# Performance work log

Measured on AMD Instinct MI355X. Metric: run time of the kernel, lower is better.

The kernel has to match this reference:

```python
import jax, jax.numpy as jnp
import numpy as np


def setup_inputs() -> dict:
    key = jax.random.key(0)
    kx, ky = jax.random.split(key)
    x = jax.random.normal(kx, (4, 8192, 3), dtype=jnp.float32)
    y = jax.random.normal(ky, (4, 8192, 3), dtype=jnp.float32)
    return {"x": x, "y": y}


def _chamfer(x, y):
    # x: [B, N, D], y: [B, M, D]
    x2 = jnp.sum(x * x, axis=-1)                      # [B, N]
    y2 = jnp.sum(y * y, axis=-1)                      # [B, M]
    xy = jnp.einsum("bnd,bmd->bnm", x, y)             # [B, N, M]
    d2 = x2[:, :, None] + y2[:, None, :] - 2.0 * xy   # [B, N, M]
    d2 = jnp.maximum(d2, 0.0)
    cham_x = jnp.min(d2, axis=2).mean(axis=1)         # [B] min over M, mean over N
    cham_y = jnp.min(d2, axis=1).mean(axis=1)         # [B] min over N, mean over M
    return cham_x + cham_y                            # [B]


def reference(x, y):
    per_batch = _chamfer(x, y)
    return jnp.mean(per_batch)  # batch_reduction='mean'
```

## Files before the change

kernel.cpp:

```cpp
#include <hip/hip_runtime.h>


#define N_      8192
#define NGRP    128
#define FLT_BIG 3.0e38f

typedef float v2f __attribute__((ext_vector_type(2)));

__global__ void zero_out_kernel(float* out) { *out = 0.0f; }

static __device__ __forceinline__ void do_record_v(
    v2f pxs, v2f pys, v2f pzs, v2f wv,
    const v2f* qx, const v2f* qy, const v2f* qz,
    float* acc)
{
    #pragma unroll
    for (int j = 0; j < 4; ++j) {
        v2f td, ts;
        asm("v_pk_fma_f32 %0, %1, %2, %3"
            : "=v"(td) : "v"(qz[j]), "v"(pzs), "v"(wv));
        asm("v_pk_fma_f32 %0, %1, %2, %3 op_sel:[0,1,1] op_sel_hi:[1,0,0]"
            : "=v"(ts) : "v"(qz[j]), "v"(pzs), "v"(wv));
        asm("v_pk_fma_f32 %0, %1, %2, %0"
            : "+v"(td) : "v"(qy[j]), "v"(pys));
        asm("v_pk_fma_f32 %0, %1, %2, %0 op_sel:[0,1,0] op_sel_hi:[1,0,1]"
            : "+v"(ts) : "v"(qy[j]), "v"(pys));
        asm("v_pk_fma_f32 %0, %1, %2, %0"
            : "+v"(td) : "v"(qx[j]), "v"(pxs));
        asm("v_pk_fma_f32 %0, %1, %2, %0 op_sel:[0,1,0] op_sel_hi:[1,0,1]"
            : "+v"(ts) : "v"(qx[j]), "v"(pxs));
        asm("v_min3_f32 %0, %0, %1, %2" : "+v"(acc[2*j])   : "v"(td.x), "v"(ts.x));
        asm("v_min3_f32 %0, %0, %1, %2" : "+v"(acc[2*j+1]) : "v"(td.y), "v"(ts.y));
    }
}

__global__ __launch_bounds__(512, 4) void chamfer_kernel(
    const float* __restrict__ xraw, const float* __restrict__ yraw,
    float* __restrict__ partial,
    unsigned int* __restrict__ ctrl,
    float* __restrict__ out)
{
    __shared__ float4 recs4[2048];
    __shared__ float  red[8 * 512];
    __shared__ unsigned int sflag;

    const int tid  = threadIdx.x;
    const int lane = tid & 63;
    const int wave = __builtin_amdgcn_readfirstlane(tid >> 6);
    const int blk  = blockIdx.x;
    const int dir   = blk >> 8;
    const int batch = (blk >> 6) & 3;
    const int qg    = (blk >> 2) & 15;
    const int seg   = blk & 3;
    const int g     = blk >> 2;

    const float* qraw = dir ? yraw : xraw;
    const float* oraw = dir ? xraw : yraw;

    {
        const float4* src4 =
            (const float4*)(oraw + (size_t)(batch * N_ + seg * 2048) * 3) + tid * 3;
        float4 a = src4[0], b = src4[1], c = src4[2];
        float w00 = fmaf(a.x, a.x, fmaf(a.y, a.y, a.z * a.z));
        float w01 = fmaf(a.w, a.w, fmaf(b.x, b.x, b.y * b.y));
        float w10 = fmaf(b.z, b.z, fmaf(b.w, b.w, c.x * c.x));
        float w11 = fmaf(c.y, c.y, fmaf(c.z, c.z, c.w * c.w));
        float4* d = &recs4[tid * 4];
        d[0] = make_float4(a.x, a.w, a.y, b.x);
        d[1] = make_float4(a.z, b.y, w00, w01);
        d[2] = make_float4(b.z, c.y, b.w, c.z);
        d[3] = make_float4(c.x, c.w, w10, w11);
    }

    const int qbase = batch * N_ + qg * 512;
    float f[24];
    {
        const float4* qv = (const float4*)(qraw + (size_t)qbase * 3) + lane * 6;
        #pragma unroll
        for (int k = 0; k < 6; ++k) {
            float4 t = qv[k];
            f[4*k] = t.x; f[4*k+1] = t.y; f[4*k+2] = t.z; f[4*k+3] = t.w;
        }
    }
    v2f qx[4], qy[4], qz[4];
    float acc[8];
    #pragma unroll
    for (int j = 0; j < 4; ++j) {
        qx[j] = (v2f){-2.0f * f[6*j+0], -2.0f * f[6*j+3]};
        qy[j] = (v2f){-2.0f * f[6*j+1], -2.0f * f[6*j+4]};
        qz[j] = (v2f){-2.0f * f[6*j+2], -2.0f * f[6*j+5]};
        acc[2*j] = FLT_BIG; acc[2*j+1] = FLT_BIG;
    }
    __syncthreads();

    const float* rp = (const float*)&recs4[wave * 256];
    #pragma unroll 4
    for (int k = 0; k < 128; ++k) {
        v2f pxs = *(const v2f*)(rp + k * 8 + 0);
        v2f pys = *(const v2f*)(rp + k * 8 + 2);
        v2f pzs = *(const v2f*)(rp + k * 8 + 4);
        v2f wv  = *(const v2f*)(rp + k * 8 + 6);
        do_record_v(pxs, pys, pzs, wv, qx, qy, qz, acc);
    }

    #pragma unroll
    for (int j = 0; j < 8; ++j) red[wave * 512 + lane * 8 + j] = acc[j];
    __syncthreads();
    float m = red[tid];
    #pragma unroll
    for (int w = 1; w < 8; ++w) m = fminf(m, red[w * 512 + tid]);

    partial[((size_t)g * 4 + seg) * 512 + tid] = m;
    __syncthreads();
    if (tid == 0) {
        __threadfence();
        sflag = atomicAdd(&ctrl[g], 1u);
    }
    __syncthreads();
    if (sflag == 3u) {
        if (tid == 0) __threadfence();
        __syncthreads();
        const float* pg = partial + (size_t)g * 4 * 512;
        float mm = fminf(fminf(pg[tid], pg[512 + tid]),
                         fminf(pg[1024 + tid], pg[1536 + tid]));
        int gq = qbase + tid;
        float ax = qraw[gq*3+0], ay = qraw[gq*3+1], az = qraw[gq*3+2];
        float qn = fmaf(ax, ax, fmaf(ay, ay, az * az));
        float d2 = fmaxf(0.0f, qn + mm);
        #pragma unroll
        for (int off = 32; off > 0; off >>= 1) d2 += __shfl_xor(d2, off);
        if (lane == 0) red[wave] = d2;
        __syncthreads();
        if (tid == 0) {
            float s = red[0];
            #pragma unroll
            for (int w = 1; w < 8; ++w) s += red[w];
            atomicAdd((float*)&ctrl[NGRP + 1], s * (1.0f / 32768.0f));
            __threadfence();
            unsigned int o2 = atomicAdd(&ctrl[NGRP], 1u);
            if (o2 == (unsigned)(NGRP - 1)) {
                float tot = atomicAdd((float*)&ctrl[NGRP + 1], 0.0f);
                *out = tot;
            }
        }
    }
}

__global__ __launch_bounds__(1024) void chamfer_raw_kernel(
    const float* __restrict__ xraw, const float* __restrict__ yraw,
    float* __restrict__ out)
{
    __shared__ float4 red4[16][64];
    const int tid  = threadIdx.x;
    const int wave = tid >> 6;
    const int lane = tid & 63;
    const int blk  = blockIdx.x;
    const bool xdir = (blk < 128);
    const int b    = (blk & 127) >> 5;
    const int qofs = (blk & 31) << 8;
    const float* qraw = xdir ? xraw : yraw;
    const float* oraw = xdir ? yraw : xraw;
    float qx0[4], qx1[4], qx2[4], acc[4];
    #pragma unroll
    for (int q = 0; q < 4; ++q) {
        int gq = b * N_ + qofs + lane*4 + q;
        qx0[q] = qraw[gq*3+0]; qx1[q] = qraw[gq*3+1]; qx2[q] = qraw[gq*3+2];
        acc[q] = FLT_BIG;
    }
    const float* opp = oraw + (size_t)(b * N_ + wave * 512) * 3;
    #pragma unroll 4
    for (int k = 0; k < 512; ++k) {
        float p0 = opp[k*3+0], p1 = opp[k*3+1], p2 = opp[k*3+2];
        float w  = fmaf(p0, p0, fmaf(p1, p1, p2*p2));
        #pragma unroll
        for (int q = 0; q < 4; ++q) {
            float dot = qx0[q]*p0 + qx1[q]*p1 + qx2[q]*p2;
            acc[q] = fminf(acc[q], fmaf(-2.0f, dot, w));
        }
    }
    red4[wave][lane] = make_float4(acc[0], acc[1], acc[2], acc[3]);
    __syncthreads();
    if (tid < 256) {
        const float* red = (const float*)red4;
        float m = red[tid];
        #pragma unroll
        for (int w = 1; w < 16; ++w) m = fminf(m, red[w*256 + tid]);
        int gq = b * N_ + qofs + tid;
        float ax = qraw[gq*3+0], ay = qraw[gq*3+1], az = qraw[gq*3+2];
        float d2 = fmaxf(0.0f, fmaf(ax,ax,fmaf(ay,ay,az*az)) + m);
        #pragma unroll
        for (int off = 32; off > 0; off >>= 1) d2 += __shfl_xor(d2, off);
        if ((tid & 63) == 0) atomicAdd(out, d2 * (1.0f / 32768.0f));
    }
}

extern "C" void kernel_launch(void* const* d_in, const int* in_sizes, int n_in,
                              void* d_out, int out_size, void* d_ws, size_t ws_size,
                              hipStream_t stream)
{
    const float* x = (const float*)d_in[0];
    const float* y = (const float*)d_in[1];
    float* out = (float*)d_out;

    const size_t need = (size_t)NGRP * 4 * 512 * sizeof(float) + (NGRP + 2) * 4;
    if (ws_size >= need) {
        float* partial = (float*)d_ws;
        unsigned int* ctrl = (unsigned int*)(partial + (size_t)NGRP * 4 * 512);
        hipMemsetAsync(ctrl, 0, (NGRP + 2) * 4, stream);
        chamfer_kernel<<<512, 512, 0, stream>>>(x, y, partial, ctrl, out);
    } else {
        zero_out_kernel<<<1, 1, 0, stream>>>(out);
        chamfer_raw_kernel<<<256, 1024, 0, stream>>>(x, y, out);
    }
}
```

Baseline: 105.6 us.

## Replace LDS staging of reference points with DPP row rotation broadcast

Drops the shared-memory staging of the opposite point cloud and the barrier that followed it. Each lane now loads one point pair straight from global memory, computes its norms in registers, and rotates the pairs across the 16-lane row with DPP row_ror, so every lane sees all 16 pairs. Loads for the next pair are prefetched before the inner loop. This removes LDS traffic and the block sync. In exchange it adds eight DPP moves per record on the VALU, which is already the busy unit in this inner loop.

```diff
diff --git a/kernel.cpp b/kernel.cpp
--- a/kernel.cpp
+++ b/kernel.cpp
@@ -2,12 +2,21 @@
 
 
 #define N_      8192
+#define RPB     4096
 #define NGRP    128
 #define FLT_BIG 3.0e38f
 
 typedef float v2f __attribute__((ext_vector_type(2)));
 
 __global__ void zero_out_kernel(float* out) { *out = 0.0f; }
+
+static __device__ __forceinline__ float rot16(float v) {
+    return __uint_as_float((unsigned)__builtin_amdgcn_update_dpp(
+        0, (int)__float_as_uint(v), 0x121, 0xf, 0xf, true));
+}
+static __device__ __forceinline__ v2f rot16v(v2f v) {
+    v2f r; r.x = rot16(v.x); r.y = rot16(v.y); return r;
+}
 
 static __device__ __forceinline__ void do_record_v(
     v2f pxs, v2f pys, v2f pzs, v2f wv,
@@ -40,8 +49,7 @@
     unsigned int* __restrict__ ctrl,
     float* __restrict__ out)
 {
-    __shared__ float4 recs4[2048];
-    __shared__ float  red[8 * 512];
+    __shared__ float red[8 * 512];
     __shared__ unsigned int sflag;
 
     const int tid  = threadIdx.x;
@@ -57,21 +65,6 @@
     const float* qraw = dir ? yraw : xraw;
     const float* oraw = dir ? xraw : yraw;
 
-    {
-        const float4* src4 =
-            (const float4*)(oraw + (size_t)(batch * N_ + seg * 2048) * 3) + tid * 3;
-        float4 a = src4[0], b = src4[1], c = src4[2];
-        float w00 = fmaf(a.x, a.x, fmaf(a.y, a.y, a.z * a.z));
-        float w01 = fmaf(a.w, a.w, fmaf(b.x, b.x, b.y * b.y));
-        float w10 = fmaf(b.z, b.z, fmaf(b.w, b.w, c.x * c.x));
-        float w11 = fmaf(c.y, c.y, fmaf(c.z, c.z, c.w * c.w));
-        float4* d = &recs4[tid * 4];
-        d[0] = make_float4(a.x, a.w, a.y, b.x);
-        d[1] = make_float4(a.z, b.y, w00, w01);
-        d[2] = make_float4(b.z, c.y, b.w, c.z);
-        d[3] = make_float4(c.x, c.w, w10, w11);
-    }
-
     const int qbase = batch * N_ + qg * 512;
     float f[24];
     {
@@ -91,16 +84,30 @@
         qz[j] = (v2f){-2.0f * f[6*j+2], -2.0f * f[6*j+5]};
         acc[2*j] = FLT_BIG; acc[2*j+1] = FLT_BIG;
     }
-    __syncthreads();
-
-    const float* rp = (const float*)&recs4[wave * 256];
-    #pragma unroll 4
-    for (int k = 0; k < 128; ++k) {
-        v2f pxs = *(const v2f*)(rp + k * 8 + 0);
-        v2f pys = *(const v2f*)(rp + k * 8 + 2);
-        v2f pzs = *(const v2f*)(rp + k * 8 + 4);
-        v2f wv  = *(const v2f*)(rp + k * 8 + 6);
-        do_record_v(pxs, pys, pzs, wv, qx, qy, qz, acc);
+
+    const float2* rp = (const float2*)
+        (oraw + (size_t)(batch * RPB + seg * 1024 + wave * 128 + (lane & 15)) * 6);
+    float2 A = rp[0], Bv = rp[1], Cv = rp[2];
+    #pragma unroll 1
+    for (int fl = 0; fl < 8; ++fl) {
+        v2f pxs = (v2f){A.x,  Bv.y};
+        v2f pys = (v2f){A.y,  Cv.x};
+        v2f pzs = (v2f){Bv.x, Cv.y};
+        v2f wv;
+        wv.x = fmaf(A.x,  A.x,  fmaf(A.y,  A.y,  Bv.x * Bv.x));
+        wv.y = fmaf(Bv.y, Bv.y, fmaf(Cv.x, Cv.x, Cv.y * Cv.y));
+        if (fl < 7) {
+            const float2* np = rp + (fl + 1) * 48;
+            A = np[0]; Bv = np[1]; Cv = np[2];
+        }
+        #pragma unroll
+        for (int s = 0; s < 16; ++s) {
+            if (s) {
+                pxs = rot16v(pxs); pys = rot16v(pys);
+                pzs = rot16v(pzs); wv  = rot16v(wv);
+            }
+            do_record_v(pxs, pys, pzs, wv, qx, qy, qz, acc);
+        }
     }
 
     #pragma unroll
@@ -128,7 +135,7 @@
         float qn = fmaf(ax, ax, fmaf(ay, ay, az * az));
         float d2 = fmaxf(0.0f, qn + mm);
         #pragma unroll
-        for (int off = 32; off > 0; off >>= 1) d2 += __shfl_xor(d2, off);
+        for (int o = 32; o > 0; o >>= 1) d2 += __shfl_xor(d2, o);
         if (lane == 0) red[wave] = d2;
         __syncthreads();
         if (tid == 0) {
```

New measurement: 111.2 us. 1.05x slower.
